# Kernel tuning notes

Hardware: AMD Instinct MI355X
Metric: run time of the kernel (lower is better)

## Reference

```python
import jax, jax.numpy as jnp
import numpy as np

B, T, D, H = 4, 2048, 1024, 16
HD = D // H


def setup_inputs() -> dict:
    key = jax.random.key(0)
    ks = jax.random.split(key, 6)
    s = 0.02
    return {
        "x": jax.random.normal(ks[0], (B, T, D), dtype=jnp.float32),
        "padding_mask": jnp.zeros((B, T), dtype=bool),
        "Wq": jax.random.normal(ks[1], (D, D), dtype=jnp.float32) * s,
        "Wk": jax.random.normal(ks[2], (D, D), dtype=jnp.float32) * s,
        "Wv": jax.random.normal(ks[3], (D, D), dtype=jnp.float32) * s,
        "Wo": jax.random.normal(ks[4], (D, D), dtype=jnp.float32) * s,
        "bo": jax.random.normal(ks[5], (D,), dtype=jnp.float32) * s,
    }


def reference(x, padding_mask, Wq, Wk, Wv, Wo, bo):
    # torch nn.Linear: y = x @ W.T
    b, t, d = x.shape
    q = (x @ Wq.T).reshape(b, t, H, HD).transpose(0, 2, 1, 3)  # [B,H,T,hd]
    k = (x @ Wk.T).reshape(b, t, H, HD).transpose(0, 2, 1, 3)
    v = (x @ Wv.T).reshape(b, t, H, HD).transpose(0, 2, 1, 3)

    scores = jnp.einsum("bhid,bhjd->bhij", q, k) / jnp.sqrt(jnp.float32(HD))
    causal = jnp.tril(jnp.ones((t, t), dtype=bool))  # [T,T]
    neg_inf = jnp.float32(-jnp.inf)
    scores = jnp.where(causal[None, None, :, :], scores, neg_inf)
    scores = jnp.where(padding_mask[:, None, None, :], neg_inf, scores)

    attn = jax.nn.softmax(scores, axis=-1)
    out = jnp.einsum("bhij,bhjd->bhid", attn, v)
    out = out.transpose(0, 2, 1, 3).reshape(b, t, d)
    out = out @ Wo.T + bo
    nonpad = (~padding_mask)[:, :, None].astype(out.dtype)
    return out * nonpad
```

## Files before the change

kernel.cpp:

```cpp
#include <hip/hip_runtime.h>

#define B_ 4
#define T_ 2048
#define D_ 1024
#define H_ 16
#define BT_ (B_ * T_)
#define QSCALE (0.125f * 1.44269504088896f)

typedef unsigned short u16;
typedef __attribute__((ext_vector_type(8))) __bf16 bf16x8;
typedef __attribute__((ext_vector_type(4))) float f32x4;

__device__ __forceinline__ u16 f2bf(float f) {
  unsigned u = __builtin_bit_cast(unsigned, f);
  u += 0x7FFFu + ((u >> 16) & 1u);
  return (u16)(u >> 16);
}

__device__ __forceinline__ void gload16(const void* g, void* l) {
  __builtin_amdgcn_global_load_lds(
      (const __attribute__((address_space(1))) void*)g,
      (__attribute__((address_space(3))) void*)l, 16, 0, 0);
}

__global__ void cvt_bf16(const float* __restrict__ in, u16* __restrict__ out, int n4) {
  int i = blockIdx.x * 256 + threadIdx.x;
  if (i >= n4) return;
  const float4 v = ((const float4*)in)[i];
  ushort4 o;
  o.x = f2bf(v.x); o.y = f2bf(v.y); o.z = f2bf(v.z); o.w = f2bf(v.w);
  ((ushort4*)out)[i] = o;
}

__global__ void pm_flags(const unsigned char* __restrict__ pm, unsigned char* __restrict__ fl) {
  int i = threadIdx.x;
  const unsigned long long* p = (const unsigned long long*)(pm + i * 64);
  unsigned long long acc = 0;
#pragma unroll
  for (int k = 0; k < 8; ++k) acc |= p[k];
  fl[i] = acc ? 1 : 0;
}

template<int MODE>
__global__ __launch_bounds__(256, 2) void gemm_bt(
    const u16* __restrict__ A, const u16* __restrict__ Bw,
    float* __restrict__ Cf, const float* __restrict__ bias,
    const unsigned char* __restrict__ rowmask,
    u16* __restrict__ Cq, u16* __restrict__ Ck, u16* __restrict__ Cvt)
{
  __shared__ __align__(16) u16 sA[128 * 64];
  __shared__ __align__(16) u16 sB[128 * 64];
  const int tid = threadIdx.x;
  const int lane = tid & 63, wave = tid >> 6;
  const int g = lane >> 4, s15 = lane & 15;
  const int bm = blockIdx.x * 128, bn = blockIdx.y * 128;
  const int wr = wave >> 1, wc = wave & 1;

  const int srow = lane >> 3;
  const int scol = ((lane & 7) ^ srow) << 3;

  f32x4 acc[4][4] = {};

  for (int kt = 0; kt < 16; ++kt) {
    __syncthreads();
    const int k0 = kt << 6;
#pragma unroll
    for (int c = 0; c < 4; ++c) {
      const int chunk = c * 4 + wave;
      gload16(A  + (size_t)(bm + chunk * 8 + srow) * 1024 + k0 + scol, (char*)sA + chunk * 1024);
      gload16(Bw + (size_t)(bn + chunk * 8 + srow) * 1024 + k0 + scol, (char*)sB + chunk * 1024);
    }
    __syncthreads();
#pragma unroll
    for (int kk = 0; kk < 2; ++kk) {
      const int cb = ((kk << 6) | (g << 4)) ^ ((s15 & 7) << 4);
      bf16x8 af[4], bf[4];
#pragma unroll
      for (int mm = 0; mm < 4; ++mm)
        af[mm] = *(const bf16x8*)((const char*)sA + (wr * 64 + mm * 16 + s15) * 128 + cb);
#pragma unroll
      for (int nn = 0; nn < 4; ++nn)
        bf[nn] = *(const bf16x8*)((const char*)sB + (wc * 64 + nn * 16 + s15) * 128 + cb);
#pragma unroll
      for (int mm = 0; mm < 4; ++mm)
#pragma unroll
        for (int nn = 0; nn < 4; ++nn)
          acc[mm][nn] = __builtin_amdgcn_mfma_f32_16x16x32_bf16(af[mm], bf[nn], acc[mm][nn], 0, 0, 0);
    }
  }

  if (MODE == 1) {
    const int region = bn >> 10;
    const float a = (region == 0) ? QSCALE : 1.f;
#pragma unroll
    for (int mm = 0; mm < 4; ++mm)
#pragma unroll
      for (int nn = 0; nn < 4; ++nn) {
        const int col = bn + wc * 64 + nn * 16 + s15;
        const int colr = col & 1023;
        const int row0 = bm + wr * 64 + mm * 16 + (g << 2);
        if (region == 2) {
          ushort4 w;
          w.x = f2bf(acc[mm][nn][0]); w.y = f2bf(acc[mm][nn][1]);
          w.z = f2bf(acc[mm][nn][2]); w.w = f2bf(acc[mm][nn][3]);
          *(ushort4*)(Cvt + (size_t)colr * BT_ + row0) = w;
        } else {
          u16* dst = region ? Ck : Cq;
#pragma unroll
          for (int r = 0; r < 4; ++r)
            dst[(size_t)(row0 + r) * 1024 + colr] = f2bf(acc[mm][nn][r] * a);
        }
      }
  } else {
#pragma unroll
    for (int mm = 0; mm < 4; ++mm)
#pragma unroll
      for (int nn = 0; nn < 4; ++nn) {
        const int col = bn + wc * 64 + nn * 16 + s15;
        const int row0 = bm + wr * 64 + mm * 16 + (g << 2);
        const float bv = bias[col];
#pragma unroll
        for (int r = 0; r < 4; ++r) {
          float v = acc[mm][nn][r] + bv;
          v = rowmask[row0 + r] ? 0.f : v;
          Cf[(size_t)(row0 + r) * 1024 + col] = v;
        }
      }
  }
}

__global__ __launch_bounds__(512, 4) void attn_fwd(
    const u16* __restrict__ Q, const u16* __restrict__ K,
    const u16* __restrict__ VT, const unsigned char* __restrict__ pm,
    const unsigned char* __restrict__ tileflag, u16* __restrict__ O)
{
  __shared__ __align__(16) u16 sK[2][64 * 64];
  __shared__ __align__(16) u16 sV[2][64 * 64];
  const int tid = threadIdx.x;
  const int lane = tid & 63, wave = tid >> 6;
  const int g = lane >> 4, s15 = lane & 15;
  const int bh = blockIdx.x, b = bh >> 4, h = bh & 15;
  const int j = blockIdx.y;
  const size_t tokbase = (size_t)b * T_;

  const int qw = (wave < 4) ? (j * 128 + wave * 32)
                            : ((15 - j) * 128 + (wave - 4) * 32);
  const int nt = 32 - 2 * j;

  const int srow = tid >> 3;
  const int sc = (tid & 7) ^ (srow & 7);
  const u16* Kb0 = K + tokbase * D_ + h * 64 + sc * 8;
  const u16* Vb0 = VT + (size_t)(h * 64) * BT_ + tokbase + sc * 8;

  bf16x8 qf[2][2];
#pragma unroll
  for (int nf = 0; nf < 2; ++nf)
#pragma unroll
    for (int ks = 0; ks < 2; ++ks)
      qf[nf][ks] = *(const bf16x8*)(Q + (tokbase + qw + nf * 16 + s15) * D_ + h * 64 + ks * 32 + g * 8);

  f32x4 o[2][4] = {};
  float l_[2] = {0.f, 0.f};

  gload16(Kb0 + (size_t)srow * D_,  (char*)(&sK[0][0]) + tid * 16);
  gload16(Vb0 + (size_t)srow * BT_, (char*)(&sV[0][0]) + tid * 16);
  __syncthreads();

  for (int t = 0; t < nt; ++t) {
    const int kv0 = t << 6;
    if (t + 1 < nt) {
      const int nb = (t + 1) & 1;
      gload16(Kb0 + (size_t)(kv0 + 64 + srow) * D_,  (char*)(&sK[nb][0]) + tid * 16);
      gload16(Vb0 + (size_t)srow * BT_ + kv0 + 64,   (char*)(&sV[nb][0]) + tid * 16);
    }

    if (kv0 <= qw + 31) {
      const u16* kb_ = &sK[t & 1][0];
      const u16* vb_ = &sV[t & 1][0];

      f32x4 st[4][2] = {};
#pragma unroll
      for (int ks = 0; ks < 2; ++ks) {
        bf16x8 kf[4];
#pragma unroll
        for (int jf = 0; jf < 4; ++jf)
          kf[jf] = *(const bf16x8*)(kb_ + (jf * 16 + s15) * 64 + (((ks * 4 + g) ^ (s15 & 7)) << 3));
        __builtin_amdgcn_s_setprio(1);
#pragma unroll
        for (int jf = 0; jf < 4; ++jf)
#pragma unroll
          for (int nf = 0; nf < 2; ++nf)
            st[jf][nf] = __builtin_amdgcn_mfma_f32_16x16x32_bf16(kf[jf], qf[nf][ks], st[jf][nf], 0, 0, 0);
        __builtin_amdgcn_s_setprio(0);
      }

#pragma unroll
      for (int nf = 0; nf < 2; ++nf) {
        if (kv0 + 63 > qw + nf * 16) {
          const int iq = qw + nf * 16 + s15;
#pragma unroll
          for (int jf = 0; jf < 4; ++jf) {
            const int jb = kv0 + jf * 16 + g * 4;
#pragma unroll
            for (int r = 0; r < 4; ++r)
              if (jb + r > iq) st[jf][nf][r] = -1e30f;
          }
        }
      }
      if (tileflag[b * 32 + t]) {
#pragma unroll
        for (int jf = 0; jf < 4; ++jf) {
          const int jb = kv0 + jf * 16 + g * 4;
          uchar4 p4 = *(const uchar4*)(pm + b * T_ + jb);
          const unsigned char* pr = (const unsigned char*)&p4;
#pragma unroll
          for (int r = 0; r < 4; ++r)
            if (pr[r]) { st[jf][0][r] = -1e30f; st[jf][1][r] = -1e30f; }
        }
      }

#pragma unroll
      for (int nf = 0; nf < 2; ++nf)
#pragma unroll
        for (int jf = 0; jf < 4; ++jf)
#pragma unroll
          for (int r = 0; r < 4; ++r) {
            const float p = __builtin_amdgcn_exp2f(st[jf][nf][r]);
            st[jf][nf][r] = p;
            l_[nf] += p;
          }

#pragma unroll
      for (int kb2 = 0; kb2 < 2; ++kb2) {
        bf16x8 vf[4];
#pragma unroll
        for (int df = 0; df < 4; ++df)
          vf[df] = *(const bf16x8*)(vb_ + (df * 16 + s15) * 64 + (((kb2 * 4 + g) ^ (s15 & 7)) << 3));
#pragma unroll
        for (int nf = 0; nf < 2; ++nf) {
          unsigned w00, w01, w10, w11;
          asm("v_cvt_pk_bf16_f32 %0, %1, %2" : "=v"(w00) : "v"(st[2*kb2][nf][0]),   "v"(st[2*kb2][nf][1]));
          asm("v_cvt_pk_bf16_f32 %0, %1, %2" : "=v"(w01) : "v"(st[2*kb2][nf][2]),   "v"(st[2*kb2][nf][3]));
          asm("v_cvt_pk_bf16_f32 %0, %1, %2" : "=v"(w10) : "v"(st[2*kb2+1][nf][0]), "v"(st[2*kb2+1][nf][1]));
          asm("v_cvt_pk_bf16_f32 %0, %1, %2" : "=v"(w11) : "v"(st[2*kb2+1][nf][2]), "v"(st[2*kb2+1][nf][3]));
          asm("v_permlane32_swap_b32 %0, %1" : "+v"(w00), "+v"(w10));
          asm("v_permlane16_swap_b32 %0, %1" : "+v"(w00), "+v"(w10));
          asm("v_permlane32_swap_b32 %0, %1" : "+v"(w01), "+v"(w11));
          asm("v_permlane16_swap_b32 %0, %1" : "+v"(w01), "+v"(w11));
          union { unsigned u[4]; bf16x8 v; } pf;
          pf.u[0] = w00; pf.u[1] = w01; pf.u[2] = w10; pf.u[3] = w11;
          __builtin_amdgcn_s_setprio(1);
#pragma unroll
          for (int df = 0; df < 4; ++df)
            o[nf][df] = __builtin_amdgcn_mfma_f32_16x16x32_bf16(vf[df], pf.v, o[nf][df], 0, 0, 0);
          __builtin_amdgcn_s_setprio(0);
        }
      }
    }
    __syncthreads();
  }

#pragma unroll
  for (int nf = 0; nf < 2; ++nf) {
    float lv = l_[nf];
    lv += __shfl_xor(lv, 16);
    lv += __shfl_xor(lv, 32);
    const float inv = 1.f / lv;
    u16* orow = O + (tokbase + qw + nf * 16 + s15) * D_ + h * 64 + g * 4;
#pragma unroll
    for (int df = 0; df < 4; ++df) {
      ushort4 w;
      w.x = f2bf(o[nf][df][0] * inv); w.y = f2bf(o[nf][df][1] * inv);
      w.z = f2bf(o[nf][df][2] * inv); w.w = f2bf(o[nf][df][3] * inv);
      *(ushort4*)(orow + df * 16) = w;
    }
  }
}

extern "C" void kernel_launch(void* const* d_in, const int* in_sizes, int n_in,
                              void* d_out, int out_size, void* d_ws, size_t ws_size,
                              hipStream_t stream)
{
  const float* x  = (const float*)d_in[0];
  const unsigned char* pm = (const unsigned char*)d_in[1];
  const float* Wq = (const float*)d_in[2];
  const float* Wk = (const float*)d_in[3];
  const float* Wv = (const float*)d_in[4];
  const float* Wo = (const float*)d_in[5];
  const float* bo = (const float*)d_in[6];
  float* out = (float*)d_out;

  char* w = (char*)d_ws;
  u16* xb  = (u16*)w; w += (size_t)BT_ * D_ * 2;
  u16* wqb = (u16*)w; w += (size_t)D_ * D_ * 2;
  u16* wkb = (u16*)w; w += (size_t)D_ * D_ * 2;
  u16* wvb = (u16*)w; w += (size_t)D_ * D_ * 2;
  u16* wob = (u16*)w; w += (size_t)D_ * D_ * 2;
  u16* qb  = (u16*)w; w += (size_t)BT_ * D_ * 2;
  u16* kbf = (u16*)w; w += (size_t)BT_ * D_ * 2;
  u16* vt  = (u16*)w; w += (size_t)BT_ * D_ * 2;
  u16* ao  = (u16*)w; w += (size_t)BT_ * D_ * 2;
  unsigned char* flags = (unsigned char*)w; w += 256;

  const int nx4 = BT_ * D_ / 4;
  const int nw4 = D_ * D_ / 4;
  cvt_bf16<<<nx4 / 256, 256, 0, stream>>>(x, xb, nx4);
  cvt_bf16<<<nw4 / 256, 256, 0, stream>>>(Wq, wqb, nw4);
  cvt_bf16<<<nw4 / 256, 256, 0, stream>>>(Wk, wkb, nw4);
  cvt_bf16<<<nw4 / 256, 256, 0, stream>>>(Wv, wvb, nw4);
  cvt_bf16<<<nw4 / 256, 256, 0, stream>>>(Wo, wob, nw4);
  pm_flags<<<1, 128, 0, stream>>>(pm, flags);

  gemm_bt<1><<<dim3(64, 24), 256, 0, stream>>>(xb, wqb, nullptr, nullptr, nullptr, qb, kbf, vt);

  attn_fwd<<<dim3(B_ * H_, 8), 512, 0, stream>>>(qb, kbf, vt, pm, flags, ao);

  gemm_bt<0><<<dim3(64, 8), 256, 0, stream>>>(ao, wob, out, bo, pm, nullptr, nullptr, nullptr);
}
```

Measured before the change: 154.5 us.

## Interleave attention query rows across waves and fuse weight conversion launches

Each of the eight waves in the attention kernel now owns one 16-row query slice from the early half and one from the late half, instead of four waves per half owning 32 rows each. The aim is to balance causal work across waves so fewer sit idle at the per-tile barrier, with per-slice activity flags skipping masked MFMAs. The row-sum is now kept as a vector accumulator. Separately, the four weight conversions and the padding-flag kernel are merged into one launch to cut launch overhead.

```diff
diff --git a/kernel.cpp b/kernel.cpp
--- a/kernel.cpp
+++ b/kernel.cpp
@@ -32,13 +32,26 @@
   ((ushort4*)out)[i] = o;
 }
 
-__global__ void pm_flags(const unsigned char* __restrict__ pm, unsigned char* __restrict__ fl) {
-  int i = threadIdx.x;
-  const unsigned long long* p = (const unsigned long long*)(pm + i * 64);
-  unsigned long long acc = 0;
-#pragma unroll
-  for (int k = 0; k < 8; ++k) acc |= p[k];
-  fl[i] = acc ? 1 : 0;
+__global__ void cvt_wts(const float* __restrict__ Wq, const float* __restrict__ Wk,
+                        const float* __restrict__ Wv, const float* __restrict__ Wo,
+                        u16* __restrict__ wdst,
+                        const unsigned char* __restrict__ pm, unsigned char* __restrict__ fl) {
+  const int by = blockIdx.y;
+  if (by < 4) {
+    const float* src = (by == 0) ? Wq : (by == 1) ? Wk : (by == 2) ? Wv : Wo;
+    const int i = blockIdx.x * 256 + threadIdx.x;
+    const float4 v = ((const float4*)src)[i];
+    ushort4 o;
+    o.x = f2bf(v.x); o.y = f2bf(v.y); o.z = f2bf(v.z); o.w = f2bf(v.w);
+    ((ushort4*)(wdst + (size_t)by * D_ * D_))[i] = o;
+  } else if (blockIdx.x == 0 && threadIdx.x < 128) {
+    const int i = threadIdx.x;
+    const unsigned long long* p = (const unsigned long long*)(pm + i * 64);
+    unsigned long long acc = 0;
+#pragma unroll
+    for (int k = 0; k < 8; ++k) acc |= p[k];
+    fl[i] = acc ? 1 : 0;
+  }
 }
 
 template<int MODE>
@@ -143,8 +156,8 @@
   const int j = blockIdx.y;
   const size_t tokbase = (size_t)b * T_;
 
-  const int qw = (wave < 4) ? (j * 128 + wave * 32)
-                            : ((15 - j) * 128 + (wave - 4) * 32);
+  const int qw0 = j * 128 + wave * 16;
+  const int qw1 = (15 - j) * 128 + wave * 16;
   const int nt = 32 - 2 * j;
 
   const int srow = tid >> 3;
@@ -154,13 +167,13 @@
 
   bf16x8 qf[2][2];
 #pragma unroll
-  for (int nf = 0; nf < 2; ++nf)
-#pragma unroll
-    for (int ks = 0; ks < 2; ++ks)
-      qf[nf][ks] = *(const bf16x8*)(Q + (tokbase + qw + nf * 16 + s15) * D_ + h * 64 + ks * 32 + g * 8);
+  for (int ks = 0; ks < 2; ++ks) {
+    qf[0][ks] = *(const bf16x8*)(Q + (tokbase + qw0 + s15) * D_ + h * 64 + ks * 32 + g * 8);
+    qf[1][ks] = *(const bf16x8*)(Q + (tokbase + qw1 + s15) * D_ + h * 64 + ks * 32 + g * 8);
+  }
 
   f32x4 o[2][4] = {};
-  float l_[2] = {0.f, 0.f};
+  f32x4 l4[2] = {};
 
   gload16(Kb0 + (size_t)srow * D_,  (char*)(&sK[0][0]) + tid * 16);
   gload16(Vb0 + (size_t)srow * BT_, (char*)(&sV[0][0]) + tid * 16);
@@ -174,99 +187,117 @@
       gload16(Vb0 + (size_t)srow * BT_ + kv0 + 64,   (char*)(&sV[nb][0]) + tid * 16);
     }
 
-    if (kv0 <= qw + 31) {
-      const u16* kb_ = &sK[t & 1][0];
-      const u16* vb_ = &sV[t & 1][0];
-
-      f32x4 st[4][2] = {};
-#pragma unroll
-      for (int ks = 0; ks < 2; ++ks) {
-        bf16x8 kf[4];
+    const bool act0 = (kv0 <= qw0 + 15);
+    const bool act1 = (kv0 <= qw1 + 15);
+    const u16* kb_ = &sK[t & 1][0];
+    const u16* vb_ = &sV[t & 1][0];
+
+    f32x4 st[4][2] = {};
+#pragma unroll
+    for (int ks = 0; ks < 2; ++ks) {
+      bf16x8 kf[4];
+#pragma unroll
+      for (int jf = 0; jf < 4; ++jf)
+        kf[jf] = *(const bf16x8*)(kb_ + (jf * 16 + s15) * 64 + (((ks * 4 + g) ^ (s15 & 7)) << 3));
+      __builtin_amdgcn_s_setprio(1);
+      if (act0)
 #pragma unroll
         for (int jf = 0; jf < 4; ++jf)
-          kf[jf] = *(const bf16x8*)(kb_ + (jf * 16 + s15) * 64 + (((ks * 4 + g) ^ (s15 & 7)) << 3));
+          st[jf][0] = __builtin_amdgcn_mfma_f32_16x16x32_bf16(kf[jf], qf[0][ks], st[jf][0], 0, 0, 0);
+      if (act1)
+#pragma unroll
+        for (int jf = 0; jf < 4; ++jf)
+          st[jf][1] = __builtin_amdgcn_mfma_f32_16x16x32_bf16(kf[jf], qf[1][ks], st[jf][1], 0, 0, 0);
+      __builtin_amdgcn_s_setprio(0);
+    }
+
+    if (act0 && kv0 + 63 > qw0) {
+      const int iq = qw0 + s15;
+#pragma unroll
+      for (int jf = 0; jf < 4; ++jf) {
+        const int jb = kv0 + jf * 16 + g * 4;
+#pragma unroll
+        for (int r = 0; r < 4; ++r)
+          if (jb + r > iq) st[jf][0][r] = -1e30f;
+      }
+    }
+    if (act1 && kv0 + 63 > qw1) {
+      const int iq = qw1 + s15;
+#pragma unroll
+      for (int jf = 0; jf < 4; ++jf) {
+        const int jb = kv0 + jf * 16 + g * 4;
+#pragma unroll
+        for (int r = 0; r < 4; ++r)
+          if (jb + r > iq) st[jf][1][r] = -1e30f;
+      }
+    }
+    if (tileflag[b * 32 + t]) {
+#pragma unroll
+      for (int jf = 0; jf < 4; ++jf) {
+        const int jb = kv0 + jf * 16 + g * 4;
+        uchar4 p4 = *(const uchar4*)(pm + b * T_ + jb);
+        const unsigned char* pr = (const unsigned char*)&p4;
+#pragma unroll
+        for (int r = 0; r < 4; ++r)
+          if (pr[r]) { st[jf][0][r] = -1e30f; st[jf][1][r] = -1e30f; }
+      }
+    }
+
+    if (act0)
+#pragma unroll
+      for (int jf = 0; jf < 4; ++jf) {
+#pragma unroll
+        for (int r = 0; r < 4; ++r)
+          st[jf][0][r] = __builtin_amdgcn_exp2f(st[jf][0][r]);
+        l4[0] += st[jf][0];
+      }
+    if (act1)
+#pragma unroll
+      for (int jf = 0; jf < 4; ++jf) {
+#pragma unroll
+        for (int r = 0; r < 4; ++r)
+          st[jf][1][r] = __builtin_amdgcn_exp2f(st[jf][1][r]);
+        l4[1] += st[jf][1];
+      }
+
+#pragma unroll
+    for (int kb2 = 0; kb2 < 2; ++kb2) {
+      bf16x8 vf[4];
+#pragma unroll
+      for (int df = 0; df < 4; ++df)
+        vf[df] = *(const bf16x8*)(vb_ + (df * 16 + s15) * 64 + (((kb2 * 4 + g) ^ (s15 & 7)) << 3));
+#pragma unroll
+      for (int nf = 0; nf < 2; ++nf) {
+        if (nf == 0 ? !act0 : !act1) continue;
+        unsigned w00, w01, w10, w11;
+        asm("v_cvt_pk_bf16_f32 %0, %1, %2" : "=v"(w00) : "v"(st[2*kb2][nf][0]),   "v"(st[2*kb2][nf][1]));
+        asm("v_cvt_pk_bf16_f32 %0, %1, %2" : "=v"(w01) : "v"(st[2*kb2][nf][2]),   "v"(st[2*kb2][nf][3]));
+        asm("v_cvt_pk_bf16_f32 %0, %1, %2" : "=v"(w10) : "v"(st[2*kb2+1][nf][0]), "v"(st[2*kb2+1][nf][1]));
+        asm("v_cvt_pk_bf16_f32 %0, %1, %2" : "=v"(w11) : "v"(st[2*kb2+1][nf][2]), "v"(st[2*kb2+1][nf][3]));
+        asm("v_permlane32_swap_b32 %0, %1" : "+v"(w00), "+v"(w10));
+        asm("v_permlane16_swap_b32 %0, %1" : "+v"(w00), "+v"(w10));
+        asm("v_permlane32_swap_b32 %0, %1" : "+v"(w01), "+v"(w11));
+        asm("v_permlane16_swap_b32 %0, %1" : "+v"(w01), "+v"(w11));
+        union { unsigned u[4]; bf16x8 v; } pf;
+        pf.u[0] = w00; pf.u[1] = w01; pf.u[2] = w10; pf.u[3] = w11;
         __builtin_amdgcn_s_setprio(1);
 #pragma unroll
-        for (int jf = 0; jf < 4; ++jf)
-#pragma unroll
-          for (int nf = 0; nf < 2; ++nf)
-            st[jf][nf] = __builtin_amdgcn_mfma_f32_16x16x32_bf16(kf[jf], qf[nf][ks], st[jf][nf], 0, 0, 0);
+        for (int df = 0; df < 4; ++df)
+          o[nf][df] = __builtin_amdgcn_mfma_f32_16x16x32_bf16(vf[df], pf.v, o[nf][df], 0, 0, 0);
         __builtin_amdgcn_s_setprio(0);
       }
-
-#pragma unroll
-      for (int nf = 0; nf < 2; ++nf) {
-        if (kv0 + 63 > qw + nf * 16) {
-          const int iq = qw + nf * 16 + s15;
-#pragma unroll
-          for (int jf = 0; jf < 4; ++jf) {
-            const int jb = kv0 + jf * 16 + g * 4;
-#pragma unroll
-            for (int r = 0; r < 4; ++r)
-              if (jb + r > iq) st[jf][nf][r] = -1e30f;
-          }
-        }
-      }
-      if (tileflag[b * 32 + t]) {
-#pragma unroll
-        for (int jf = 0; jf < 4; ++jf) {
-          const int jb = kv0 + jf * 16 + g * 4;
-          uchar4 p4 = *(const uchar4*)(pm + b * T_ + jb);
-          const unsigned char* pr = (const unsigned char*)&p4;
-#pragma unroll
-          for (int r = 0; r < 4; ++r)
-            if (pr[r]) { st[jf][0][r] = -1e30f; st[jf][1][r] = -1e30f; }
-        }
-      }
-
-#pragma unroll
-      for (int nf = 0; nf < 2; ++nf)
-#pragma unroll
-        for (int jf = 0; jf < 4; ++jf)
-#pragma unroll
-          for (int r = 0; r < 4; ++r) {
-            const float p = __builtin_amdgcn_exp2f(st[jf][nf][r]);
-            st[jf][nf][r] = p;
-            l_[nf] += p;
-          }
-
-#pragma unroll
-      for (int kb2 = 0; kb2 < 2; ++kb2) {
-        bf16x8 vf[4];
-#pragma unroll
-        for (int df = 0; df < 4; ++df)
-          vf[df] = *(const bf16x8*)(vb_ + (df * 16 + s15) * 64 + (((kb2 * 4 + g) ^ (s15 & 7)) << 3));
-#pragma unroll
-        for (int nf = 0; nf < 2; ++nf) {
-          unsigned w00, w01, w10, w11;
-          asm("v_cvt_pk_bf16_f32 %0, %1, %2" : "=v"(w00) : "v"(st[2*kb2][nf][0]),   "v"(st[2*kb2][nf][1]));
-          asm("v_cvt_pk_bf16_f32 %0, %1, %2" : "=v"(w01) : "v"(st[2*kb2][nf][2]),   "v"(st[2*kb2][nf][3]));
-          asm("v_cvt_pk_bf16_f32 %0, %1, %2" : "=v"(w10) : "v"(st[2*kb2+1][nf][0]), "v"(st[2*kb2+1][nf][1]));
-          asm("v_cvt_pk_bf16_f32 %0, %1, %2" : "=v"(w11) : "v"(st[2*kb2+1][nf][2]), "v"(st[2*kb2+1][nf][3]));
-          asm("v_permlane32_swap_b32 %0, %1" : "+v"(w00), "+v"(w10));
-          asm("v_permlane16_swap_b32 %0, %1" : "+v"(w00), "+v"(w10));
-          asm("v_permlane32_swap_b32 %0, %1" : "+v"(w01), "+v"(w11));
-          asm("v_permlane16_swap_b32 %0, %1" : "+v"(w01), "+v"(w11));
-          union { unsigned u[4]; bf16x8 v; } pf;
-          pf.u[0] = w00; pf.u[1] = w01; pf.u[2] = w10; pf.u[3] = w11;
-          __builtin_amdgcn_s_setprio(1);
-#pragma unroll
-          for (int df = 0; df < 4; ++df)
-            o[nf][df] = __builtin_amdgcn_mfma_f32_16x16x32_bf16(vf[df], pf.v, o[nf][df], 0, 0, 0);
-          __builtin_amdgcn_s_setprio(0);
-        }
-      }
     }
     __syncthreads();
   }
 
 #pragma unroll
   for (int nf = 0; nf < 2; ++nf) {
-    float lv = l_[nf];
+    float lv = (l4[nf][0] + l4[nf][1]) + (l4[nf][2] + l4[nf][3]);
     lv += __shfl_xor(lv, 16);
     lv += __shfl_xor(lv, 32);
     const float inv = 1.f / lv;
-    u16* orow = O + (tokbase + qw + nf * 16 + s15) * D_ + h * 64 + g * 4;
+    const int qw = nf ? qw1 : qw0;
+    u16* orow = O + (tokbase + qw + s15) * D_ + h * 64 + g * 4;
 #pragma unroll
     for (int df = 0; df < 4; ++df) {
       ushort4 w;
@@ -301,15 +332,11 @@
   u16* vt  = (u16*)w; w += (size_t)BT_ * D_ * 2;
   u16* ao  = (u16*)w; w += (size_t)BT_ * D_ * 2;
   unsigned char* flags = (unsigned char*)w; w += 256;
+  (void)wkb; (void)wvb;
 
   const int nx4 = BT_ * D_ / 4;
-  const int nw4 = D_ * D_ / 4;
   cvt_bf16<<<nx4 / 256, 256, 0, stream>>>(x, xb, nx4);
-  cvt_bf16<<<nw4 / 256, 256, 0, stream>>>(Wq, wqb, nw4);
-  cvt_bf16<<<nw4 / 256, 256, 0, stream>>>(Wk, wkb, nw4);
-  cvt_bf16<<<nw4 / 256, 256, 0, stream>>>(Wv, wvb, nw4);
-  cvt_bf16<<<nw4 / 256, 256, 0, stream>>>(Wo, wob, nw4);
-  pm_flags<<<1, 128, 0, stream>>>(pm, flags);
+  cvt_wts<<<dim3(1024, 5), 256, 0, stream>>>(Wq, Wk, Wv, Wo, wqb, pm, flags);
 
   gemm_bt<1><<<dim3(64, 24), 256, 0, stream>>>(xb, wqb, nullptr, nullptr, nullptr, qb, kbf, vt);
 
```

After: 143.9 us. 6.8% less time.
